# Kernel optimization log

Measured on AMD Instinct MI355X. Metric: run time of the kernel, lower is better.

## Reference

```python
import jax, jax.numpy as jnp
import numpy as np

N = 500_000       # nodes
E = 8_000_000     # edges (avg degree 16)
IN_DIM = 16       # node_in_dim
HID = 32          # DCRNN hidden (hard-coded in RecurrentGCN)
OUT_DIM = 8       # node_out_dim


def setup_inputs() -> dict:
    key = jax.random.key(0)
    ks = jax.random.split(key, 12)
    scale_g = 1.0 / np.sqrt(IN_DIM + HID)  # glorot-ish for DConv weights
    scale_l = 1.0 / np.sqrt(HID)
    return {
        "x": jax.random.normal(ks[0], (N, IN_DIM), jnp.float32),
        "edge_index": jax.random.randint(ks[1], (2, E), 0, N, jnp.int32),
        "edge_weight": jax.random.uniform(ks[2], (E,), jnp.float32),
        "h": jnp.zeros((N, HID), jnp.float32),
        # DConv weights: original shape (2, K=1, in, out); K=1 -> store (2, in, out)
        "w_z": jax.random.normal(ks[3], (2, IN_DIM + HID, HID), jnp.float32) * scale_g,
        "b_z": jnp.zeros((HID,), jnp.float32),
        "w_r": jax.random.normal(ks[4], (2, IN_DIM + HID, HID), jnp.float32) * scale_g,
        "b_r": jnp.zeros((HID,), jnp.float32),
        "w_h": jax.random.normal(ks[5], (2, IN_DIM + HID, HID), jnp.float32) * scale_g,
        "b_h": jnp.zeros((HID,), jnp.float32),
        "w_lin": jax.random.normal(ks[6], (HID, OUT_DIM), jnp.float32) * scale_l,
        "b_lin": jnp.zeros((OUT_DIM,), jnp.float32),
    }


def _dconv_k1(xh, w, b):
    # DConv with K=1: only the Chebyshev k=0 term survives:
    #   H = X @ W[0,0] + X @ W[1,0] + b  (out-diffusion + in-diffusion weights)
    # edge_index / edge_weight do not enter the math for K=1.
    return xh @ (w[0] + w[1]) + b


def reference(x, edge_index, edge_weight, h, w_z, b_z, w_r, b_r, w_h, b_h, w_lin, b_lin):
    # DCRNN GRU cell (h=None in torch -> zeros, supplied explicitly here)
    xh = jnp.concatenate([x, h], axis=1)                  # [N, IN+HID]
    z = jax.nn.sigmoid(_dconv_k1(xh, w_z, b_z))           # update gate [N, HID]
    r = jax.nn.sigmoid(_dconv_k1(xh, w_r, b_r))           # reset gate  [N, HID]
    xhr = jnp.concatenate([x, h * r], axis=1)             # [N, IN+HID]
    h_tilde = jnp.tanh(_dconv_k1(xhr, w_h, b_h))          # candidate   [N, HID]
    h_new = z * h + (1.0 - z) * h_tilde                   # [N, HID]
    out = jax.nn.relu(h_new) @ w_lin + b_lin              # [N, OUT_DIM]
    return (out, h_new)
```

## Files before the change

kernel.cpp:

```cpp
#include <hip/hip_runtime.h>


#define N_NODES 500000
#define IN_DIM  16
#define HID     32
#define OUT_DIM 8
#define XH      48
#define NTILES  31250

typedef unsigned int u32;
typedef unsigned short u16;
typedef __attribute__((ext_vector_type(8))) short bf16x8;
typedef __attribute__((ext_vector_type(4))) float f32x4;

static __device__ __forceinline__ float bfbits(u32 hi){ union{u32 x; float f;} t; t.x=hi; return t.f; }
static __device__ __forceinline__ float bflo(u32 u){ return bfbits(u<<16); }
static __device__ __forceinline__ float bfhi(u32 u){ return bfbits(u & 0xffff0000u); }
static __device__ __forceinline__ float bf2f(u16 s){ return bfbits(((u32)s)<<16); }
static __device__ __forceinline__ u16 f2bf(float f){
    union{float f;u32 x;} t; t.f=f; u32 x=t.x;
    return (u16)((x + 0x7fffu + ((x>>16)&1u)) >> 16);
}
static __device__ __forceinline__ u32 pk2(float a, float b){
    return (u32)f2bf(a) | ((u32)f2bf(b)<<16);
}
static __device__ __forceinline__ float sigm(float a){
    a = fminf(fmaxf(a,-30.f),30.f); return 1.f/(1.f+__expf(-a));
}
static __device__ __forceinline__ float tanh_(float a){
    a = fminf(fmaxf(a,-20.f),20.f); float e = __expf(-2.f*a); return (1.f-e)/(1.f+e);
}

#define LFENCE() asm volatile("s_waitcnt lgkmcnt(0)" ::: "memory")
#define MFMA16(a,b,c) __builtin_amdgcn_mfma_f32_16x16x32_bf16(a,b,c,0,0,0)

static __device__ __forceinline__ float ldf(const void* p, int i, bool F32){
    return F32 ? ((const float*)p)[i] : bf2f(((const u16*)p)[i]);
}
static __device__ __forceinline__ float wsum(const void* wp, int k, int c, bool F32){
    int i0 = k*HID + c;
    return ldf(wp, i0, F32) + ldf(wp, XH*HID + i0, F32);
}
static __device__ __forceinline__ char* stgp(char* base, int row, int off){
    return base + row*128 + (off ^ ((row & 7) << 4));
}

__global__ __launch_bounds__(256)
void rgcn_kernel(const void* __restrict__ xp_,
                 const void* __restrict__ hp_,
                 const void* __restrict__ wz_, const void* __restrict__ bz_,
                 const void* __restrict__ wr_, const void* __restrict__ br_,
                 const void* __restrict__ wh_, const void* __restrict__ bh_,
                 const void* __restrict__ wl_, const void* __restrict__ bl_,
                 void* __restrict__ dout_)
{
    __shared__ u16   sStage[4][16*64];
    __shared__ float sHf[4][16*36];
    __shared__ float sOut[4][16*8];
    __shared__ int sF32;

    const int tid = threadIdx.x;

    if (tid == 0) {
        const u32* xw = (const u32*)xp_;
        int f = 0;
        for (int q = 0; q < 128; q++) {
            float lo = bflo(xw[q]);
            if (!(fabsf(lo) <= 1e6f)) { f = 1; break; }
        }
        sF32 = f;
    }
    __syncthreads();
    const bool F32 = (sF32 != 0);

    const int lane = tid & 63, wv = tid >> 6;
    const int c16 = lane & 15, g = lane >> 4;
    const int row4 = lane >> 2, q4 = lane & 3;
    char*  stage = (char*)sStage[wv];
    float* hf    = sHf[wv];
    float* obuf  = sOut[wv];

    {
        uint2 z2; z2.x = 0u; z2.y = 0u;
        *(uint2*)stgp(stage, row4, 96 + q4*8) = z2;
    }

    float bzv[2], brv[2], bhv[2];
#pragma unroll
    for (int tt = 0; tt < 2; tt++) {
        bzv[tt] = ldf(bz_, c16 + 16*tt, F32);
        brv[tt] = ldf(br_, c16 + 16*tt, F32);
        bhv[tt] = ldf(bh_, c16 + 16*tt, F32);
    }
    float blv = (c16 < OUT_DIM) ? ldf(bl_, c16, F32) : 0.f;

    bf16x8 Bz[2][2], Br[2][2], Bh[2][2], Bl;
#pragma unroll
    for (int kt = 0; kt < 2; kt++) {
#pragma unroll
        for (int tt = 0; tt < 2; tt++) {
            union { u16 us[8]; bf16x8 v; } uz, ur, uh;
#pragma unroll
            for (int e = 0; e < 8; e++) {
                int k = kt*32 + g*8 + e;
                int c = c16 + 16*tt;
                float vz = 0.f, vr = 0.f, vh = 0.f;
                if (k < XH) {
                    vz = wsum(wz_, k, c, F32);
                    vr = wsum(wr_, k, c, F32);
                    vh = wsum(wh_, k, c, F32);
                }
                uz.us[e] = f2bf(vz); ur.us[e] = f2bf(vr); uh.us[e] = f2bf(vh);
            }
            Bz[kt][tt] = uz.v; Br[kt][tt] = ur.v; Bh[kt][tt] = uh.v;
        }
    }
    {
        union { u16 us[8]; bf16x8 v; } ul;
#pragma unroll
        for (int e = 0; e < 8; e++) {
            int k = g*8 + e;
            float v = (c16 < OUT_DIM) ? ldf(wl_, k*OUT_DIM + c16, F32) : 0.f;
            ul.us[e] = f2bf(v);
        }
        Bl = ul.v;
    }

    const int wid = blockIdx.x*4 + wv;
    const int nw  = gridDim.x*4;

    for (int t = wid; t < NTILES; t += nw) {
        const size_t nb = (size_t)t * 16;

        if (F32) {
            const float* xb = (const float*)xp_ + nb*IN_DIM;
            float4 xv = *(const float4*)(xb + row4*IN_DIM + q4*4);
            uint2 xp2; xp2.x = pk2(xv.x, xv.y); xp2.y = pk2(xv.z, xv.w);
            *(uint2*)stgp(stage, row4, q4*8) = xp2;
            const float* hb = (const float*)hp_ + nb*HID;
            float4 h0 = *(const float4*)(hb + row4*HID + q4*8);
            float4 h1 = *(const float4*)(hb + row4*HID + q4*8 + 4);
            uint4 hp4; hp4.x = pk2(h0.x,h0.y); hp4.y = pk2(h0.z,h0.w);
            hp4.z = pk2(h1.x,h1.y); hp4.w = pk2(h1.z,h1.w);
            *(uint4*)stgp(stage, row4, 32 + q4*16) = hp4;
            *(float4*)(hf + row4*36 + q4*8)     = h0;
            *(float4*)(hf + row4*36 + q4*8 + 4) = h1;
        } else {
            const u16* xb = (const u16*)xp_ + nb*IN_DIM;
            uint2 xv = *(const uint2*)(xb + row4*IN_DIM + q4*4);
            *(uint2*)stgp(stage, row4, q4*8) = xv;
            const u16* hb = (const u16*)hp_ + nb*HID;
            uint4 hv = *(const uint4*)(hb + row4*HID + q4*8);
            *(uint4*)stgp(stage, row4, 32 + q4*16) = hv;
            float4 e0, e1;
            e0.x = bflo(hv.x); e0.y = bfhi(hv.x); e0.z = bflo(hv.y); e0.w = bfhi(hv.y);
            e1.x = bflo(hv.z); e1.y = bfhi(hv.z); e1.z = bflo(hv.w); e1.w = bfhi(hv.w);
            *(float4*)(hf + row4*36 + q4*8)     = e0;
            *(float4*)(hf + row4*36 + q4*8 + 4) = e1;
        }
        LFENCE();

        bf16x8 a0 = *(const bf16x8*)stgp(stage, c16, g*16);
        bf16x8 a1 = *(const bf16x8*)stgp(stage, c16, 64 + g*16);

        f32x4 accZ[2], accR[2];
#pragma unroll
        for (int tt = 0; tt < 2; tt++) {
            f32x4 az; az[0]=bzv[tt]; az[1]=bzv[tt]; az[2]=bzv[tt]; az[3]=bzv[tt];
            az = MFMA16(a0, Bz[0][tt], az);
            az = MFMA16(a1, Bz[1][tt], az);
            accZ[tt] = az;
            f32x4 ar; ar[0]=brv[tt]; ar[1]=brv[tt]; ar[2]=brv[tt]; ar[3]=brv[tt];
            ar = MFMA16(a0, Br[0][tt], ar);
            ar = MFMA16(a1, Br[1][tt], ar);
            accR[tt] = ar;
        }

        float hvv[2][4], zz[2][4];
#pragma unroll
        for (int tt = 0; tt < 2; tt++) {
#pragma unroll
            for (int rr = 0; rr < 4; rr++) {
                int nl = g*4 + rr;
                float hcur = hf[nl*36 + c16 + 16*tt];
                hvv[tt][rr] = hcur;
                zz[tt][rr]  = sigm(accZ[tt][rr]);
                float rv    = sigm(accR[tt][rr]);
                *(u16*)stgp(stage, nl, 32 + 2*c16 + 32*tt) = f2bf(hcur * rv);
            }
        }
        LFENCE();

        bf16x8 b0 = *(const bf16x8*)stgp(stage, c16, g*16);
        bf16x8 b1 = *(const bf16x8*)stgp(stage, c16, 64 + g*16);
        f32x4 accH[2];
#pragma unroll
        for (int tt = 0; tt < 2; tt++) {
            f32x4 ah; ah[0]=bhv[tt]; ah[1]=bhv[tt]; ah[2]=bhv[tt]; ah[3]=bhv[tt];
            ah = MFMA16(b0, Bh[0][tt], ah);
            ah = MFMA16(b1, Bh[1][tt], ah);
            accH[tt] = ah;
        }

#pragma unroll
        for (int tt = 0; tt < 2; tt++) {
#pragma unroll
            for (int rr = 0; rr < 4; rr++) {
                int nl = g*4 + rr;
                float ht = tanh_(accH[tt][rr]);
                float z  = zz[tt][rr];
                float hn = z*hvv[tt][rr] + (1.f - z)*ht;
                hf[nl*36 + c16 + 16*tt] = hn;
                *(u16*)stgp(stage, nl, 2*c16 + 32*tt) = f2bf(fmaxf(hn, 0.f));
            }
        }
        LFENCE();

        bf16x8 a3 = *(const bf16x8*)stgp(stage, c16, g*16);
        f32x4 accO; accO[0]=blv; accO[1]=blv; accO[2]=blv; accO[3]=blv;
        accO = MFMA16(a3, Bl, accO);
        if (c16 < OUT_DIM) {
#pragma unroll
            for (int rr = 0; rr < 4; rr++) obuf[(g*4+rr)*OUT_DIM + c16] = accO[rr];
        }
        LFENCE();

        if (F32) {
            float* outp = (float*)dout_;
            float* hnp  = outp + (size_t)N_NODES*OUT_DIM;
            float4 s0 = *(const float4*)(hf + row4*36 + q4*8);
            float4 s1 = *(const float4*)(hf + row4*36 + q4*8 + 4);
            float* hd = hnp + (nb + row4)*HID + q4*8;
            *(float4*)hd = s0; *(float4*)(hd+4) = s1;
            if (lane < 32) {
                float4 o = *(const float4*)(obuf + (lane>>1)*OUT_DIM + (lane&1)*4);
                *(float4*)(outp + (nb + (lane>>1))*OUT_DIM + (lane&1)*4) = o;
            }
        } else {
            u16* outp = (u16*)dout_;
            u16* hnp  = outp + (size_t)N_NODES*OUT_DIM;
            float4 s0 = *(const float4*)(hf + row4*36 + q4*8);
            float4 s1 = *(const float4*)(hf + row4*36 + q4*8 + 4);
            uint4 pv; pv.x = pk2(s0.x,s0.y); pv.y = pk2(s0.z,s0.w);
            pv.z = pk2(s1.x,s1.y); pv.w = pk2(s1.z,s1.w);
            *(uint4*)(hnp + (nb + row4)*HID + q4*8) = pv;
            if (lane < 16) {
                float4 o0 = *(const float4*)(obuf + lane*OUT_DIM);
                float4 o1 = *(const float4*)(obuf + lane*OUT_DIM + 4);
                uint4 ov; ov.x = pk2(o0.x,o0.y); ov.y = pk2(o0.z,o0.w);
                ov.z = pk2(o1.x,o1.y); ov.w = pk2(o1.z,o1.w);
                *(uint4*)(outp + (nb + lane)*OUT_DIM) = ov;
            }
        }
    }
}

extern "C" void kernel_launch(void* const* d_in, const int* in_sizes, int n_in,
                              void* d_out, int out_size, void* d_ws, size_t ws_size,
                              hipStream_t stream) {
    const int block = 256;
    const int grid  = 2048;
    rgcn_kernel<<<grid, block, 0, stream>>>(
        d_in[0], d_in[3], d_in[4], d_in[5], d_in[6], d_in[7],
        d_in[8], d_in[9], d_in[10], d_in[11], d_out);
}
```

Baseline: 258.2 us.

## Interleave hidden columns per lane, store outputs directly, use hardware bf16 pack

Each lane now owns adjacent hidden column pairs (2*c16+tt) instead of columns c16 and c16+16. This lets the gate math read h and write h*r and relu(h_new) as packed 32-bit pairs, and write h_new straight to global memory as float2 or u32. The LDS output buffer and the final restaging pass are removed, and output rows are written directly from the MFMA accumulators. Software bf16 rounding is replaced with v_cvt_pk_bf16_f32, and the clamps in sigmoid and tanh are dropped. The cost is global stores that are narrower and more scattered (8-byte h_new and 4-byte out stores instead of 16-byte vectors), which could hurt store coalescing.

Result: no change. 262.0 us (+1.5%).

```diff
diff --git a/kernel.cpp b/kernel.cpp
--- a/kernel.cpp
+++ b/kernel.cpp
@@ -7,6 +7,7 @@
 #define OUT_DIM 8
 #define XH      48
 #define NTILES  31250
+#define HFS     36
 
 typedef unsigned int u32;
 typedef unsigned short u16;
@@ -21,14 +22,16 @@
     union{float f;u32 x;} t; t.f=f; u32 x=t.x;
     return (u16)((x + 0x7fffu + ((x>>16)&1u)) >> 16);
 }
-static __device__ __forceinline__ u32 pk2(float a, float b){
-    return (u32)f2bf(a) | ((u32)f2bf(b)<<16);
+static __device__ __forceinline__ u32 cvtpk(float a, float b){
+    u32 r; asm("v_cvt_pk_bf16_f32 %0, %1, %2" : "=v"(r) : "v"(a), "v"(b)); return r;
 }
 static __device__ __forceinline__ float sigm(float a){
-    a = fminf(fmaxf(a,-30.f),30.f); return 1.f/(1.f+__expf(-a));
+    return 1.f / (1.f + __expf(-a));
 }
 static __device__ __forceinline__ float tanh_(float a){
-    a = fminf(fmaxf(a,-20.f),20.f); float e = __expf(-2.f*a); return (1.f-e)/(1.f+e);
+    float e = __expf(-2.f * fabsf(a));
+    float t = (1.f - e) / (1.f + e);
+    return __builtin_copysignf(t, a);
 }
 
 #define LFENCE() asm volatile("s_waitcnt lgkmcnt(0)" ::: "memory")
@@ -55,8 +58,7 @@
                  void* __restrict__ dout_)
 {
     __shared__ u16   sStage[4][16*64];
-    __shared__ float sHf[4][16*36];
-    __shared__ float sOut[4][16*8];
+    __shared__ float sHf[4][16*HFS];
     __shared__ int sF32;
 
     const int tid = threadIdx.x;
@@ -78,7 +80,20 @@
     const int row4 = lane >> 2, q4 = lane & 3;
     char*  stage = (char*)sStage[wv];
     float* hf    = sHf[wv];
-    float* obuf  = sOut[wv];
+
+    char* pXw = stgp(stage, row4, q4*8);
+    char* pHw = stgp(stage, row4, 32 + q4*16);
+    float* pHfw = hf + row4*HFS + q4*8;
+    char* pA0 = stgp(stage, c16, 16*g);
+    char* pA1 = stgp(stage, c16, 64 + 16*g);
+    char* pPairH[4]; char* pPairR[4]; const float* pHfr[4];
+#pragma unroll
+    for (int rr = 0; rr < 4; rr++) {
+        int nl = g*4 + rr;
+        pPairH[rr] = stgp(stage, nl, 32 + 4*c16);
+        pPairR[rr] = stgp(stage, nl, 4*c16);
+        pHfr[rr]   = hf + nl*HFS + 2*c16;
+    }
 
     {
         uint2 z2; z2.x = 0u; z2.y = 0u;
@@ -88,9 +103,9 @@
     float bzv[2], brv[2], bhv[2];
 #pragma unroll
     for (int tt = 0; tt < 2; tt++) {
-        bzv[tt] = ldf(bz_, c16 + 16*tt, F32);
-        brv[tt] = ldf(br_, c16 + 16*tt, F32);
-        bhv[tt] = ldf(bh_, c16 + 16*tt, F32);
+        bzv[tt] = ldf(bz_, 2*c16 + tt, F32);
+        brv[tt] = ldf(br_, 2*c16 + tt, F32);
+        bhv[tt] = ldf(bh_, 2*c16 + tt, F32);
     }
     float blv = (c16 < OUT_DIM) ? ldf(bl_, c16, F32) : 0.f;
 
@@ -103,7 +118,7 @@
 #pragma unroll
             for (int e = 0; e < 8; e++) {
                 int k = kt*32 + g*8 + e;
-                int c = c16 + 16*tt;
+                int c = 2*c16 + tt;
                 float vz = 0.f, vr = 0.f, vh = 0.f;
                 if (k < XH) {
                     vz = wsum(wz_, k, c, F32);
@@ -126,6 +141,11 @@
         Bl = ul.v;
     }
 
+    float* outF = (float*)dout_;
+    float* hnF  = outF + (size_t)N_NODES * OUT_DIM;
+    u16*   outB = (u16*)dout_;
+    u16*   hnB  = outB + (size_t)N_NODES * OUT_DIM;
+
     const int wid = blockIdx.x*4 + wv;
     const int nw  = gridDim.x*4;
 
@@ -135,33 +155,25 @@
         if (F32) {
             const float* xb = (const float*)xp_ + nb*IN_DIM;
             float4 xv = *(const float4*)(xb + row4*IN_DIM + q4*4);
-            uint2 xp2; xp2.x = pk2(xv.x, xv.y); xp2.y = pk2(xv.z, xv.w);
-            *(uint2*)stgp(stage, row4, q4*8) = xp2;
+            uint2 xp2; xp2.x = cvtpk(xv.x, xv.y); xp2.y = cvtpk(xv.z, xv.w);
+            *(uint2*)pXw = xp2;
             const float* hb = (const float*)hp_ + nb*HID;
             float4 h0 = *(const float4*)(hb + row4*HID + q4*8);
             float4 h1 = *(const float4*)(hb + row4*HID + q4*8 + 4);
-            uint4 hp4; hp4.x = pk2(h0.x,h0.y); hp4.y = pk2(h0.z,h0.w);
-            hp4.z = pk2(h1.x,h1.y); hp4.w = pk2(h1.z,h1.w);
-            *(uint4*)stgp(stage, row4, 32 + q4*16) = hp4;
-            *(float4*)(hf + row4*36 + q4*8)     = h0;
-            *(float4*)(hf + row4*36 + q4*8 + 4) = h1;
+            uint4 hp4; hp4.x = cvtpk(h0.x,h0.y); hp4.y = cvtpk(h0.z,h0.w);
+            hp4.z = cvtpk(h1.x,h1.y); hp4.w = cvtpk(h1.z,h1.w);
+            *(uint4*)pHw = hp4;
+            *(float4*)pHfw = h0; *(float4*)(pHfw + 4) = h1;
         } else {
             const u16* xb = (const u16*)xp_ + nb*IN_DIM;
-            uint2 xv = *(const uint2*)(xb + row4*IN_DIM + q4*4);
-            *(uint2*)stgp(stage, row4, q4*8) = xv;
+            *(uint2*)pXw = *(const uint2*)(xb + row4*IN_DIM + q4*4);
             const u16* hb = (const u16*)hp_ + nb*HID;
-            uint4 hv = *(const uint4*)(hb + row4*HID + q4*8);
-            *(uint4*)stgp(stage, row4, 32 + q4*16) = hv;
-            float4 e0, e1;
-            e0.x = bflo(hv.x); e0.y = bfhi(hv.x); e0.z = bflo(hv.y); e0.w = bfhi(hv.y);
-            e1.x = bflo(hv.z); e1.y = bfhi(hv.z); e1.z = bflo(hv.w); e1.w = bfhi(hv.w);
-            *(float4*)(hf + row4*36 + q4*8)     = e0;
-            *(float4*)(hf + row4*36 + q4*8 + 4) = e1;
+            *(uint4*)pHw = *(const uint4*)(hb + row4*HID + q4*8);
         }
         LFENCE();
 
-        bf16x8 a0 = *(const bf16x8*)stgp(stage, c16, g*16);
-        bf16x8 a1 = *(const bf16x8*)stgp(stage, c16, 64 + g*16);
+        bf16x8 a0 = *(const bf16x8*)pA0;
+        bf16x8 a1 = *(const bf16x8*)pA1;
 
         f32x4 accZ[2], accR[2];
 #pragma unroll
@@ -176,23 +188,27 @@
             accR[tt] = ar;
         }
 
-        float hvv[2][4], zz[2][4];
-#pragma unroll
-        for (int tt = 0; tt < 2; tt++) {
-#pragma unroll
-            for (int rr = 0; rr < 4; rr++) {
-                int nl = g*4 + rr;
-                float hcur = hf[nl*36 + c16 + 16*tt];
-                hvv[tt][rr] = hcur;
-                zz[tt][rr]  = sigm(accZ[tt][rr]);
-                float rv    = sigm(accR[tt][rr]);
-                *(u16*)stgp(stage, nl, 32 + 2*c16 + 32*tt) = f2bf(hcur * rv);
-            }
+        float z0a[4], z1a[4], hv0[4], hv1[4];
+#pragma unroll
+        for (int rr = 0; rr < 4; rr++) {
+            float h0, h1;
+            if (F32) {
+                float2 hp2 = *(const float2*)pHfr[rr];
+                h0 = hp2.x; h1 = hp2.y;
+            } else {
+                u32 hw = *(const u32*)pPairH[rr];
+                h0 = bflo(hw); h1 = bfhi(hw);
+            }
+            hv0[rr] = h0; hv1[rr] = h1;
+            float z0 = sigm(accZ[0][rr]), z1 = sigm(accZ[1][rr]);
+            z0a[rr] = z0; z1a[rr] = z1;
+            float r0 = sigm(accR[0][rr]), r1 = sigm(accR[1][rr]);
+            *(u32*)pPairH[rr] = cvtpk(h0*r0, h1*r1);
         }
         LFENCE();
 
-        bf16x8 b0 = *(const bf16x8*)stgp(stage, c16, g*16);
-        bf16x8 b1 = *(const bf16x8*)stgp(stage, c16, 64 + g*16);
+        bf16x8 b0 = *(const bf16x8*)pA0;
+        bf16x8 b1 = *(const bf16x8*)pA1;
         f32x4 accH[2];
 #pragma unroll
         for (int tt = 0; tt < 2; tt++) {
@@ -203,53 +219,33 @@
         }
 
 #pragma unroll
-        for (int tt = 0; tt < 2; tt++) {
-#pragma unroll
-            for (int rr = 0; rr < 4; rr++) {
-                int nl = g*4 + rr;
-                float ht = tanh_(accH[tt][rr]);
-                float z  = zz[tt][rr];
-                float hn = z*hvv[tt][rr] + (1.f - z)*ht;
-                hf[nl*36 + c16 + 16*tt] = hn;
-                *(u16*)stgp(stage, nl, 2*c16 + 32*tt) = f2bf(fmaxf(hn, 0.f));
+        for (int rr = 0; rr < 4; rr++) {
+            int nl = g*4 + rr;
+            float t0 = tanh_(accH[0][rr]), t1 = tanh_(accH[1][rr]);
+            float n0 = t0 + z0a[rr]*(hv0[rr] - t0);
+            float n1 = t1 + z1a[rr]*(hv1[rr] - t1);
+            *(u32*)pPairR[rr] = cvtpk(fmaxf(n0, 0.f), fmaxf(n1, 0.f));
+            if (F32) {
+                float2 st; st.x = n0; st.y = n1;
+                *(float2*)(hnF + (nb + nl)*HID + 2*c16) = st;
+            } else {
+                *(u32*)(hnB + (nb + nl)*HID + 2*c16) = cvtpk(n0, n1);
             }
         }
         LFENCE();
 
-        bf16x8 a3 = *(const bf16x8*)stgp(stage, c16, g*16);
+        bf16x8 a3 = *(const bf16x8*)pA0;
         f32x4 accO; accO[0]=blv; accO[1]=blv; accO[2]=blv; accO[3]=blv;
         accO = MFMA16(a3, Bl, accO);
         if (c16 < OUT_DIM) {
-#pragma unroll
-            for (int rr = 0; rr < 4; rr++) obuf[(g*4+rr)*OUT_DIM + c16] = accO[rr];
-        }
-        LFENCE();
-
-        if (F32) {
-            float* outp = (float*)dout_;
-            float* hnp  = outp + (size_t)N_NODES*OUT_DIM;
-            float4 s0 = *(const float4*)(hf + row4*36 + q4*8);
-            float4 s1 = *(const float4*)(hf + row4*36 + q4*8 + 4);
-            float* hd = hnp + (nb + row4)*HID + q4*8;
-            *(float4*)hd = s0; *(float4*)(hd+4) = s1;
-            if (lane < 32) {
-                float4 o = *(const float4*)(obuf + (lane>>1)*OUT_DIM + (lane&1)*4);
-                *(float4*)(outp + (nb + (lane>>1))*OUT_DIM + (lane&1)*4) = o;
-            }
-        } else {
-            u16* outp = (u16*)dout_;
-            u16* hnp  = outp + (size_t)N_NODES*OUT_DIM;
-            float4 s0 = *(const float4*)(hf + row4*36 + q4*8);
-            float4 s1 = *(const float4*)(hf + row4*36 + q4*8 + 4);
-            uint4 pv; pv.x = pk2(s0.x,s0.y); pv.y = pk2(s0.z,s0.w);
-            pv.z = pk2(s1.x,s1.y); pv.w = pk2(s1.z,s1.w);
-            *(uint4*)(hnp + (nb + row4)*HID + q4*8) = pv;
-            if (lane < 16) {
-                float4 o0 = *(const float4*)(obuf + lane*OUT_DIM);
-                float4 o1 = *(const float4*)(obuf + lane*OUT_DIM + 4);
-                uint4 ov; ov.x = pk2(o0.x,o0.y); ov.y = pk2(o0.z,o0.w);
-                ov.z = pk2(o1.x,o1.y); ov.w = pk2(o1.z,o1.w);
-                *(uint4*)(outp + (nb + lane)*OUT_DIM) = ov;
+            if (F32) {
+#pragma unroll
+                for (int rr = 0; rr < 4; rr++)
+                    outF[(nb + g*4 + rr)*OUT_DIM + c16] = accO[rr];
+            } else {
+#pragma unroll
+                for (int rr = 0; rr < 4; rr++)
+                    outB[(nb + g*4 + rr)*OUT_DIM + c16] = (u16)(cvtpk(accO[rr], accO[rr]) & 0xffffu);
             }
         }
     }
```
